# Optimization experiments

Hardware: AMD Instinct MI355X
Metric: run time of the kernel (lower is better)

## Reference

```python
import jax, jax.numpy as jnp
import numpy as np

B, DIM, HEADS, H, W, WS, AWS = 8, 64, 4, 256, 256, 8, 8
HD = DIM // HEADS
SCALE = HD ** -0.5


def _grid_sample_zeros(img, grid):
    # img: (N, C, Hi, Wi); grid: (N, Ho, Wo, 2) with (x, y) in [-1, 1]
    # bilinear, align_corners=True, zero padding (matches F.grid_sample)
    N, C, Hi, Wi = img.shape
    gx = (grid[..., 0] + 1.0) * 0.5 * (Wi - 1)
    gy = (grid[..., 1] + 1.0) * 0.5 * (Hi - 1)
    x0 = jnp.floor(gx).astype(jnp.int32); x1 = x0 + 1
    y0 = jnp.floor(gy).astype(jnp.int32); y1 = y0 + 1
    wx1 = gx - x0; wx0 = 1.0 - wx1
    wy1 = gy - y0; wy0 = 1.0 - wy1

    def one(im, x0, x1, y0, y1, wx0, wx1, wy0, wy1):
        def g(yi, xi):
            valid = ((yi >= 0) & (yi < Hi) & (xi >= 0) & (xi < Wi)).astype(im.dtype)
            v = im[:, jnp.clip(yi, 0, Hi - 1), jnp.clip(xi, 0, Wi - 1)]
            return v * valid[None]
        return (g(y0, x0) * (wy0 * wx0)[None] + g(y0, x1) * (wy0 * wx1)[None]
                + g(y1, x0) * (wy1 * wx0)[None] + g(y1, x1) * (wy1 * wx1)[None])

    return jax.vmap(one)(img, x0, x1, y0, y1, wx0, wx1, wy0, wy1)


def _rel_index():
    c = np.stack(np.meshgrid(np.arange(AWS), np.arange(AWS), indexing='ij'))
    cf = c.reshape(2, -1)
    rel = (cf[:, :, None] - cf[:, None, :]).transpose(1, 2, 0).copy()
    rel[:, :, 0] += AWS - 1
    rel[:, :, 1] += AWS - 1
    rel[:, :, 0] *= 2 * AWS - 1
    return rel.sum(-1)  # (AWS*AWS, AWS*AWS)


_REL_IDX = jnp.asarray(_rel_index())


def setup_inputs():
    key = jax.random.key(0)
    ks = jax.random.split(key, 8)
    s = 0.02
    return {
        'x': jax.random.normal(ks[0], (B, DIM, H, W), jnp.float32),
        'qkv_w': jax.random.normal(ks[1], (3 * DIM, DIM), jnp.float32) * s,
        'qkv_b': jnp.zeros((3 * DIM,), jnp.float32),
        'proj_w': jax.random.normal(ks[2], (DIM, DIM), jnp.float32) * s,
        'proj_b': jnp.zeros((DIM,), jnp.float32),
        'off_w': jax.random.normal(ks[3], (2 * HEADS, DIM), jnp.float32) * s,
        'off_b': jnp.zeros((2 * HEADS,), jnp.float32),
        'sc_w': jax.random.normal(ks[4], (2 * HEADS, DIM), jnp.float32) * s,
        'sc_b': jnp.zeros((2 * HEADS,), jnp.float32),
        'rel_bias': jax.random.normal(ks[5], ((WS + AWS - 1) ** 2, HEADS), jnp.float32) * s,
    }


def reference(x, qkv_w, qkv_b, proj_w, proj_b, off_w, off_b, sc_w, sc_b, rel_bias):
    b, dim, h, w = x.shape
    pad_td = (WS - h % WS) % WS; pad_lr = (WS - w % WS) % WS
    pt, pd = pad_td // 2, pad_td - pad_td // 2
    pl, pr = pad_lr // 2, pad_lr - pad_lr // 2
    eh, ew = h + pad_td, w + pad_lr
    wnh, wnw = eh // WS, ew // WS

    # per-pixel reference grid in [-1,1]; channel 0 = x(w-axis), channel 1 = y(h-axis)
    ref_h = jnp.linspace(-1.0, 1.0, eh)
    ref_w = jnp.linspace(-1.0, 1.0, ew)
    base = jnp.stack([jnp.broadcast_to(ref_w[None, :], (eh, ew)),
                      jnp.broadcast_to(ref_h[:, None], (eh, ew))], 0)
    base = base.reshape(2, wnh, WS, wnw, WS)

    # zero-mean window-relative attention coordinates
    bch = jnp.arange(AWS, dtype=jnp.float32) * 2 * WS / AWS / (eh - 1); bch = bch - bch.mean()
    bcw = jnp.arange(AWS, dtype=jnp.float32) * 2 * WS / AWS / (ew - 1); bcw = bcw - bcw.mean()
    ech = jnp.tile(bch, wnh)
    ecw = jnp.tile(bcw, wnw)
    wc = jnp.stack([jnp.broadcast_to(ecw[None, :], (wnh * AWS, wnw * AWS)),
                    jnp.broadcast_to(ech[:, None], (wnh * AWS, wnw * AWS))], 0)
    wc = wc.reshape(2, wnh, AWS, wnw, AWS)

    xp = jnp.pad(x, ((0, 0), (0, 0), (pt, pd), (pl, pr)))

    # offsets / scales: avgpool(WS) -> leaky_relu -> 1x1 conv
    pooled = xp.reshape(b, dim, wnh, WS, wnw, WS).mean(axis=(3, 5))
    act = jax.nn.leaky_relu(pooled, 0.01)
    off = jnp.einsum('bchw,oc->bohw', act, off_w) + off_b[None, :, None, None]
    off = off.reshape(b * HEADS, 2, wnh, wnw)
    off = off * jnp.array([1.0 / (h // WS), 1.0 / (w // WS)], off.dtype)[None, :, None, None]
    sc = jnp.einsum('bchw,oc->bohw', act, sc_w) + sc_b[None, :, None, None]
    sc = sc.reshape(b * HEADS, 2, wnh, wnw)

    coords = (base[None] + wc[None] * sc[:, :, :, None, :, None]
              + off[:, :, :, None, :, None])  # (b*heads, 2, wnh, AWS, wnw, AWS)
    grid = coords.transpose(0, 2, 3, 4, 5, 1).reshape(b * HEADS, wnh * AWS, wnw * AWS, 2)

    # qkv 1x1 conv, then spatial pad
    qkv = jnp.einsum('bchw,oc->bohw', x, qkv_w) + qkv_b[None, :, None, None]
    qkv = qkv.reshape(b, 3, HEADS, HD, h, w)
    qkv = jnp.pad(qkv, ((0, 0),) * 4 + ((pt, pd), (pl, pr)))
    q = qkv[:, 0].reshape(b * HEADS, HD, eh, ew)
    k = qkv[:, 1].reshape(b * HEADS, HD, eh, ew)
    v = qkv[:, 2].reshape(b * HEADS, HD, eh, ew)

    k_sel = _grid_sample_zeros(k, grid)
    v_sel = _grid_sample_zeros(v, grid)

    q = q.reshape(b, HEADS, HD, wnh, WS, wnw, WS).transpose(0, 3, 5, 1, 4, 6, 2)
    q = q.reshape(b * wnh * wnw, HEADS, WS * WS, HD)

    def to_win(t):
        t = t.reshape(b, HEADS, HD, wnh, AWS, wnw, AWS).transpose(0, 3, 5, 1, 4, 6, 2)
        return t.reshape(b * wnh * wnw, HEADS, AWS * AWS, HD)

    kw, vw = to_win(k_sel), to_win(v_sel)

    dots = jnp.einsum('wnqd,wnkd->wnqk', q, kw) * SCALE
    bias = rel_bias[_REL_IDX]  # (WS*WS, AWS*AWS, HEADS)
    dots = dots + bias.transpose(2, 0, 1)[None]
    attn = jax.nn.softmax(dots, axis=-1)
    out = jnp.einsum('wnqk,wnkd->wnqd', attn, vw)

    out = out.reshape(b, wnh, wnw, HEADS, WS, WS, HD).transpose(0, 3, 6, 1, 4, 2, 5)
    out = out.reshape(b, dim, eh, ew)[:, :, pt:h + pt, pl:w + pl]
    out = jnp.einsum('bchw,oc->bohw', out, proj_w) + proj_b[None, :, None, None]
    return out
```

## Files before the change

### kernel.cpp

```cpp
#include <hip/hip_runtime.h>

#define BATCH 8
#define CDIM 64
#define NHEADS 4
#define HD 16
#define IMG 256
#define WSZ 8
#define WN 32
#define NWIN (WN * WN)

static constexpr size_t OFFSC_FLOATS = (size_t)BATCH * NHEADS * NWIN * 4;
static constexpr size_t MAP_ELEMS = (size_t)BATCH * NHEADS * IMG * IMG * HD;

typedef unsigned short u16;
typedef __attribute__((ext_vector_type(2))) _Float16 h2;
typedef __attribute__((ext_vector_type(8))) _Float16 h8;
typedef __attribute__((ext_vector_type(4))) float f32x4;

__device__ __forceinline__ unsigned cvt_pk_f16(float a, float b) {
    unsigned r;
    asm("v_cvt_pkrtz_f16_f32 %0, %1, %2" : "=v"(r) : "v"(a), "v"(b));
    return r;
}
__device__ __forceinline__ float rcpf(float s) {
    float r;
    asm("v_rcp_f32 %0, %1" : "=v"(r) : "v"(s));
    return r;
}
union UH2 { unsigned u; h2 h; };
__device__ __forceinline__ h2 u2h2(unsigned u) { UH2 x; x.u = u; return x.h; }
__device__ __forceinline__ unsigned h22u(h2 h) { UH2 x; x.h = h; return x.u; }
__device__ __forceinline__ u16 f2h(float f) {
    _Float16 h = (_Float16)f;
    u16 r;
    __builtin_memcpy(&r, &h, 2);
    return r;
}
__device__ __forceinline__ unsigned pk_rne(float a, float b) {
    return (unsigned)f2h(a) | ((unsigned)f2h(b) << 16);
}

#define DPP_RADD(x, ctrl)                                                         \
    x += __int_as_float(__builtin_amdgcn_update_dpp(                              \
        0, __float_as_int(x), (ctrl), 0xF, 0xF, false))

__global__ __launch_bounds__(256) void k_pool(const float* __restrict__ x,
                                              float* __restrict__ actg,
                                              const float* __restrict__ qkv_w,
                                              const float* __restrict__ proj_w,
                                              unsigned* __restrict__ wbf) {
    __shared__ float red[8][8][33];
    int bid = blockIdx.x;
    int cg = bid & 7, wh = (bid >> 3) & 31, b = bid >> 8;
    int t = threadIdx.x;
    int row = t >> 5, colg = t & 31;

    if (bid < 32) {
        int i = bid * 256 + t;
        if (i < 6144) {
            wbf[i] = cvt_pk_f16(qkv_w[2 * i], qkv_w[2 * i + 1]);
        } else {
            int j = i - 6144;
            wbf[i] = cvt_pk_f16(proj_w[2 * j], proj_w[2 * j + 1]);
        }
    }

    const float* xb = x + (((size_t)(b * CDIM + cg * 8) * IMG) + (size_t)(wh * WSZ + row)) * IMG + colg * 8;
    #pragma unroll
    for (int c = 0; c < 8; c++) {
        const float4* p4 = (const float4*)(xb + (size_t)c * IMG * IMG);
        float4 a = p4[0], bq = p4[1];
        red[c][row][colg] = a.x + a.y + a.z + a.w + bq.x + bq.y + bq.z + bq.w;
    }
    __syncthreads();
    int c = t >> 5, ww = t & 31;
    float s = 0.f;
    #pragma unroll
    for (int r = 0; r < 8; r++) s += red[c][r][ww];
    s *= (1.0f / 64.0f);
    s = (s >= 0.f) ? s : 0.01f * s;
    actg[(((size_t)b * CDIM + cg * 8 + c) * WN + wh) * WN + ww] = s;
}

__global__ __launch_bounds__(256) void k_offmv(const float* __restrict__ actg,
                                               const float* __restrict__ off_w,
                                               const float* __restrict__ off_b,
                                               const float* __restrict__ sc_w,
                                               const float* __restrict__ sc_b,
                                               float* __restrict__ offsc) {
    __shared__ float act[CDIM][WN + 1];
    int b = blockIdx.x >> 5, wh = blockIdx.x & 31;
    int t = threadIdx.x;
    for (int i = t; i < CDIM * WN; i += 256) {
        int c = i >> 5, ww = i & 31;
        act[c][ww] = actg[(((size_t)b * CDIM + c) * WN + wh) * WN + ww];
    }
    __syncthreads();
    int ww = t >> 3, oi = t & 7;
    float ao = off_b[oi], as = sc_b[oi];
    #pragma unroll 8
    for (int c = 0; c < CDIM; c++) {
        float av = act[c][ww];
        ao += av * off_w[oi * CDIM + c];
        as += av * sc_w[oi * CDIM + c];
    }
    ao *= (1.0f / 32.0f);
    int n = oi >> 1, d = oi & 1;
    size_t base = (((size_t)(b * NHEADS + n) * NWIN) + wh * WN + ww) << 2;
    offsc[base + d] = ao;
    offsc[base + 2 + d] = as;
}

__global__ __launch_bounds__(256) void k_qkv_mfma(const float* __restrict__ x,
                                                  const u16* __restrict__ wbf,
                                                  const float* __restrict__ qkv_b,
                                                  u16* __restrict__ qm,
                                                  u16* __restrict__ km,
                                                  u16* __restrict__ vm) {
    __shared__ u16 Alds[256 * 64];

    int bid = blockIdx.x;
    bid = (bid & 7) * 256 + (bid >> 3);
    int b = bid >> 8, y = bid & 255;
    int t = threadIdx.x;

    {
        const float* xp = x + ((size_t)b * CDIM * IMG + y) * IMG + t;
        u16* row = Alds + t * 64;
        int sw = t & 7;
        #pragma unroll
        for (int cp = 0; cp < 32; cp++) {
            float a = xp[(size_t)(2 * cp) * IMG * IMG];
            float bq = xp[(size_t)(2 * cp + 1) * IMG * IMG];
            unsigned pk = cvt_pk_f16(a, bq);
            int c = 2 * cp;
            int chunk = c >> 3;
            *(unsigned*)(row + ((chunk ^ sw) << 3) + (c & 7)) = pk;
        }
    }

    int wv = t >> 6, l = t & 63;
    int lr = l & 15, lg = l >> 4;

    h8 afr[4][2];
    #pragma unroll
    for (int pg = 0; pg < 4; pg++) {
        int p = wv * 64 + pg * 16 + lr;
        const u16* prow = Alds + p * 64;
        int psw = p & 7;
        #pragma unroll
        for (int kb = 0; kb < 2; kb++) {
            int chunk = kb * 4 + lg;
            afr[pg][kb] = *(const h8*)(prow + ((chunk ^ psw) << 3));
        }
    }

    u16* const maps[3] = { qm, km, vm };
    #pragma unroll
    for (int ot = 0; ot < 12; ot++) {
        int o = ot * 16 + lr;
        float4 b4 = *(const float4*)(qkv_b + ot * 16 + lg * 4);
        h8 bfr0 = *(const h8*)(wbf + o * 64 + lg * 8);
        h8 bfr1 = *(const h8*)(wbf + o * 64 + 32 + lg * 8);

        f32x4 acc[4];
        #pragma unroll
        for (int pg = 0; pg < 4; pg++) {
            acc[pg] = (f32x4){ b4.x, b4.y, b4.z, b4.w };
            acc[pg] = __builtin_amdgcn_mfma_f32_16x16x32_f16(bfr0, afr[pg][0], acc[pg], 0, 0, 0);
            acc[pg] = __builtin_amdgcn_mfma_f32_16x16x32_f16(bfr1, afr[pg][1], acc[pg], 0, 0, 0);
        }

        u16* mp = maps[ot >> 2];
        int n = ot & 3;
        size_t base = ((size_t)(b * NHEADS + n) * IMG * IMG + (size_t)y * IMG) * HD;
        #pragma unroll
        for (int pg = 0; pg < 4; pg++) {
            size_t sb = base + (size_t)(wv * 64 + pg * 16 + lr) * HD + lg * 4;
            *(uint2*)(mp + sb) = make_uint2(pk_rne(acc[pg][0], acc[pg][1]),
                                            pk_rne(acc[pg][2], acc[pg][3]));
        }
    }
}

__global__ __launch_bounds__(256, 2) void k_attn3(const u16* __restrict__ qm,
                                                  const u16* __restrict__ km,
                                                  const u16* __restrict__ vm,
                                                  const u16* __restrict__ wproj,
                                                  const float* __restrict__ proj_b,
                                                  const float* __restrict__ rel_bias,
                                                  const float* __restrict__ offsc,
                                                  float* __restrict__ out) {
    __shared__ float biasS[NHEADS * 225];
    __shared__ _Float16 hb[NHEADS][2048];
    _Float16* Ob = &hb[0][0];

    int blk = blockIdx.x;
    blk = (blk & 7) * 1024 + (blk >> 3);
    int b = blk >> 10, wh = (blk >> 5) & 31, ww = blk & 31;
    int tid = threadIdx.x, n = tid >> 6, l = tid & 63;
    int g = l >> 4, cl = l & 15;
    int y0 = wh * WSZ, x0 = ww * WSZ;
    const h8 z8 = {};

    for (int i = tid; i < NHEADS * 225; i += 256) {
        int hn = i / 225, idx = i - hn * 225;
        biasS[i] = rel_bias[idx * NHEADS + hn] * 4.0f;
    }

    float4 os4 = *(const float4*)(offsc + ((((size_t)(b * NHEADS + n) * NWIN) + wh * WN + ww) << 2));

    h8 qfr[4];
    {
        const u16* qb = qm + ((size_t)(b * NHEADS + n) << 16) * HD;
        #pragma unroll
        for (int qt = 0; qt < 4; qt++) {
            int q = qt * 16 + cl;
            qfr[qt] = (g < 2)
                ? *(const h8*)(qb + ((size_t)(y0 + (q >> 3)) * IMG + (x0 + (q & 7))) * HD + g * 8)
                : z8;
        }
    }

    h8 wfr[2];
    #pragma unroll
    for (int h = 0; h < 2; h++)
        wfr[h] = *(const h8*)(wproj + (n * 16 + cl) * 64 + h * 32 + g * 8);
    float4 pb4 = *(const float4*)(proj_b + n * 16 + g * 4);

    {
        float offx = os4.x, offy = os4.y;
        float scx = os4.z, scy = os4.w;
        int pi = l >> 3, pj = l & 7;
        float gx = (float)(x0 + pj) + ((float)(2 * pj - 7) * (1.0f / 255.0f) * scx + offx) * 127.5f;
        float gy = (float)(y0 + pi) + ((float)(2 * pi - 7) * (1.0f / 255.0f) * scy + offy) * 127.5f;

        float fx0 = floorf(gx), fy0 = floorf(gy);
        int ix0 = (int)fx0, iy0 = (int)fy0;
        float wx1 = gx - fx0, wx0 = 1.f - wx1;
        float wy1 = gy - fy0, wy0 = 1.f - wy1;

        const u16* kb = km + ((size_t)(b * NHEADS + n) << 16) * HD;
        const u16* vb = vm + ((size_t)(b * NHEADS + n) << 16) * HD;

        int iys[2] = { iy0, iy0 + 1 };
        int ixs[2] = { ix0, ix0 + 1 };
        float wys[2] = { wy0, wy1 };
        float wxs[2] = { wx0, wx1 };

        size_t offs[4];
        h2 w2[4];
        #pragma unroll
        for (int t = 0; t < 4; t++) {
            int yy = iys[t >> 1], xq = ixs[t & 1];
            float wgt = wys[t >> 1] * wxs[t & 1];
            if (yy < 0 || yy >= IMG || xq < 0 || xq >= IMG) wgt = 0.f;
            int yc = min(max(yy, 0), IMG - 1), xc = min(max(xq, 0), IMG - 1);
            offs[t] = ((size_t)yc * IMG + xc) * HD;
            _Float16 hw = (_Float16)wgt;
            w2[t] = (h2){ hw, hw };
        }

        h2 kacc[8], vacc[8];
        #pragma unroll
        for (int i = 0; i < 8; i++) {
            kacc[i] = (h2){ (_Float16)0, (_Float16)0 };
            vacc[i] = (h2){ (_Float16)0, (_Float16)0 };
        }

        {
            uint4 t0[4], t1[4];
            #pragma unroll
            for (int t = 0; t < 4; t++) {
                const uint4* p = (const uint4*)(kb + offs[t]);
                t0[t] = p[0]; t1[t] = p[1];
            }
            #pragma unroll
            for (int t = 0; t < 4; t++) {
                kacc[0] += w2[t] * u2h2(t0[t].x); kacc[1] += w2[t] * u2h2(t0[t].y);
                kacc[2] += w2[t] * u2h2(t0[t].z); kacc[3] += w2[t] * u2h2(t0[t].w);
                kacc[4] += w2[t] * u2h2(t1[t].x); kacc[5] += w2[t] * u2h2(t1[t].y);
                kacc[6] += w2[t] * u2h2(t1[t].z); kacc[7] += w2[t] * u2h2(t1[t].w);
            }
        }
        {
            uint4 t0[4], t1[4];
            #pragma unroll
            for (int t = 0; t < 4; t++) {
                const uint4* p = (const uint4*)(vb + offs[t]);
                t0[t] = p[0]; t1[t] = p[1];
            }
            #pragma unroll
            for (int t = 0; t < 4; t++) {
                vacc[0] += w2[t] * u2h2(t0[t].x); vacc[1] += w2[t] * u2h2(t0[t].y);
                vacc[2] += w2[t] * u2h2(t0[t].z); vacc[3] += w2[t] * u2h2(t0[t].w);
                vacc[4] += w2[t] * u2h2(t1[t].x); vacc[5] += w2[t] * u2h2(t1[t].y);
                vacc[6] += w2[t] * u2h2(t1[t].z); vacc[7] += w2[t] * u2h2(t1[t].w);
            }
        }

        uint4* kp = (uint4*)(&hb[n][0] + (size_t)l * 16);
        kp[0] = make_uint4(h22u(kacc[0]), h22u(kacc[1]), h22u(kacc[2]), h22u(kacc[3]));
        kp[1] = make_uint4(h22u(kacc[4]), h22u(kacc[5]), h22u(kacc[6]), h22u(kacc[7]));

        int p = cl * 4 + g;
        #pragma unroll
        for (int i = 0; i < 8; i++) {
            int d0 = 2 * i, d1 = 2 * i + 1;
            hb[n][1024 + d0 * 64 + (p ^ ((d0 & 3) << 4))] = vacc[i][0];
            hb[n][1024 + d1 * 64 + (p ^ ((d1 & 3) << 4))] = vacc[i][1];
        }
    }

    h8 kfr[4], vfr[2];
    #pragma unroll
    for (int kt = 0; kt < 4; kt++)
        kfr[kt] = (g < 2) ? *(const h8*)(&hb[n][0] + (kt * 16 + cl) * 16 + g * 8) : z8;
    #pragma unroll
    for (int h = 0; h < 2; h++)
        vfr[h] = *(const h8*)(&hb[n][1024] + cl * 64 + ((h * 32 + g * 8) ^ ((cl & 3) << 4)));

    __syncthreads();

    f32x4 dacc[4][4];
    #pragma unroll
    for (int qt = 0; qt < 4; qt++) {
        #pragma unroll
        for (int kt = 0; kt < 4; kt++) {
            int pik = kt * 2 + (cl >> 3), pjk = cl & 7;
            int bidx = n * 225 + (7 - pik) * 15 + (7 - pjk) + (qt * 2 + (g >> 1)) * 15 + (g & 1) * 4;
            f32x4 c = { biasS[bidx], biasS[bidx + 1], biasS[bidx + 2], biasS[bidx + 3] };
            dacc[qt][kt] = __builtin_amdgcn_mfma_f32_16x16x32_f16(qfr[qt], kfr[kt], c, 0, 0, 0);
        }
    }

    _Float16* Pb = &hb[n][0];
    f32x4 oacc[4];
    float inv_[4][4];
    #pragma unroll
    for (int qt = 0; qt < 4; qt++) {
        #pragma unroll
        for (int kt = 0; kt < 4; kt++)
            #pragma unroll
            for (int r = 0; r < 4; r++)
                dacc[qt][kt][r] = exp2f(dacc[qt][kt][r] * 0.36067376f);
        #pragma unroll
        for (int r = 0; r < 4; r++) {
            float s0 = (dacc[qt][0][r] + dacc[qt][1][r]) + (dacc[qt][2][r] + dacc[qt][3][r]);
            DPP_RADD(s0, 0x121);
            DPP_RADD(s0, 0x122);
            DPP_RADD(s0, 0x124);
            DPP_RADD(s0, 0x128);
            inv_[qt][r] = rcpf(s0);
        }
        #pragma unroll
        for (int r = 0; r < 4; r++) {
            unsigned lo = cvt_pk_f16(dacc[qt][0][r], dacc[qt][1][r]);
            unsigned hi = cvt_pk_f16(dacc[qt][2][r], dacc[qt][3][r]);
            *(uint2*)((u16*)Pb + (g * 4 + r) * 64 + ((cl * 4) ^ (r << 4))) = make_uint2(lo, hi);
        }
        f32x4 pv = { 0.f, 0.f, 0.f, 0.f };
        #pragma unroll
        for (int h = 0; h < 2; h++) {
            h8 af = *(const h8*)(Pb + cl * 64 + ((h * 32 + g * 8) ^ ((cl & 3) << 4)));
            pv = __builtin_amdgcn_mfma_f32_16x16x32_f16(af, vfr[h], pv, 0, 0, 0);
        }
        oacc[qt] = pv;
    }

    __syncthreads();

    #pragma unroll
    for (int qt = 0; qt < 4; qt++)
        #pragma unroll
        for (int r = 0; r < 4; r++) {
            int q = qt * 16 + g * 4 + r;
            Ob[q * 64 + ((n * 16 + cl) ^ (g << 4))] = (_Float16)(oacc[qt][r] * inv_[qt][r]);
        }
    __syncthreads();

    #pragma unroll
    for (int qt = 0; qt < 4; qt++) {
        f32x4 pa = { pb4.x, pb4.y, pb4.z, pb4.w };
        #pragma unroll
        for (int h = 0; h < 2; h++) {
            h8 of = *(const h8*)(Ob + (qt * 16 + cl) * 64 + ((h * 32 + g * 8) ^ ((cl >> 2) << 4)));
            pa = __builtin_amdgcn_mfma_f32_16x16x32_f16(wfr[h], of, pa, 0, 0, 0);
        }
        int q = qt * 16 + cl;
        #pragma unroll
        for (int r = 0; r < 4; r++) {
            out[((size_t)(b * CDIM + n * 16 + g * 4 + r) * IMG + y0 + (q >> 3)) * IMG + x0 + (q & 7)] = pa[r];
        }
    }
}

extern "C" void kernel_launch(void* const* d_in, const int* in_sizes, int n_in,
                              void* d_out, int out_size, void* d_ws, size_t ws_size,
                              hipStream_t stream) {
    const float* x      = (const float*)d_in[0];
    const float* qkv_w  = (const float*)d_in[1];
    const float* qkv_b  = (const float*)d_in[2];
    const float* proj_w = (const float*)d_in[3];
    const float* proj_b = (const float*)d_in[4];
    const float* off_w  = (const float*)d_in[5];
    const float* off_b  = (const float*)d_in[6];
    const float* sc_w   = (const float*)d_in[7];
    const float* sc_b   = (const float*)d_in[8];
    const float* rel_b  = (const float*)d_in[9];
    float* out = (float*)d_out;

    float* ws = (float*)d_ws;
    float* offsc = ws;
    u16* wqkv = (u16*)(ws + OFFSC_FLOATS);
    u16* wprj = wqkv + 12288;
    u16* qmm = wprj + 4096;
    u16* kmm = qmm + MAP_ELEMS;
    u16* vmm = kmm + MAP_ELEMS;
    float* actg = (float*)qmm;

    k_pool<<<BATCH * WN * 8, 256, 0, stream>>>(x, actg, qkv_w, proj_w, (unsigned*)wqkv);
    k_offmv<<<BATCH * WN, 256, 0, stream>>>(actg, off_w, off_b, sc_w, sc_b, offsc);
    k_qkv_mfma<<<BATCH * IMG, 256, 0, stream>>>(x, wqkv, qkv_b, qmm, kmm, vmm);
    k_attn3<<<BATCH * NWIN, 256, 0, stream>>>(qmm, kmm, vmm, wprj, proj_b,
                                              rel_b, offsc, out);
}
```

Measured before the change: 225.9 us.

## Process two attention windows per block and prefetch second window's K/V gathers

Each attention block now handles two adjacent 8x8 windows instead of one. Grid size is halved, and the bias table setup and projection weight loads are amortized over both windows. The second window's bilinear K/V gathers and Q loads are issued early, behind sched barriers, so they overlap the first window's softmax and projection work. A separate shared buffer for the output tile is added. This raises register and LDS pressure, which may lower occupancy under launch_bounds(256,2).

Result: slower. 240.8 us (+6.6%).

```diff
diff --git a/kernel.cpp b/kernel.cpp
--- a/kernel.cpp
+++ b/kernel.cpp
@@ -193,14 +193,14 @@
                                                   float* __restrict__ out) {
     __shared__ float biasS[NHEADS * 225];
     __shared__ _Float16 hb[NHEADS][2048];
-    _Float16* Ob = &hb[0][0];
+    __shared__ _Float16 Ob[64 * 64];
 
     int blk = blockIdx.x;
-    blk = (blk & 7) * 1024 + (blk >> 3);
-    int b = blk >> 10, wh = (blk >> 5) & 31, ww = blk & 31;
+    blk = (blk & 7) * 512 + (blk >> 3);
+    int b = blk >> 9, wh = (blk >> 4) & 31, wp = blk & 15;
     int tid = threadIdx.x, n = tid >> 6, l = tid & 63;
     int g = l >> 4, cl = l & 15;
-    int y0 = wh * WSZ, x0 = ww * WSZ;
+    int y0 = wh * WSZ, x0a = wp * 16, x0b = wp * 16 + 8;
     const h8 z8 = {};
 
     for (int i = tid; i < NHEADS * 225; i += 256) {
@@ -208,18 +208,21 @@
         biasS[i] = rel_bias[idx * NHEADS + hn] * 4.0f;
     }
 
-    float4 os4 = *(const float4*)(offsc + ((((size_t)(b * NHEADS + n) * NWIN) + wh * WN + ww) << 2));
-
-    h8 qfr[4];
-    {
-        const u16* qb = qm + ((size_t)(b * NHEADS + n) << 16) * HD;
-        #pragma unroll
-        for (int qt = 0; qt < 4; qt++) {
-            int q = qt * 16 + cl;
-            qfr[qt] = (g < 2)
-                ? *(const h8*)(qb + ((size_t)(y0 + (q >> 3)) * IMG + (x0 + (q & 7))) * HD + g * 8)
-                : z8;
-        }
+    size_t osbase = (((size_t)(b * NHEADS + n) * NWIN) + wh * WN + wp * 2) << 2;
+    float4 osA = *(const float4*)(offsc + osbase);
+    float4 osB = *(const float4*)(offsc + osbase + 4);
+
+    const u16* qb = qm + ((size_t)(b * NHEADS + n) << 16) * HD;
+    const u16* kb = km + ((size_t)(b * NHEADS + n) << 16) * HD;
+    const u16* vb = vm + ((size_t)(b * NHEADS + n) << 16) * HD;
+
+    h8 qfrA[4];
+    #pragma unroll
+    for (int qt = 0; qt < 4; qt++) {
+        int q = qt * 16 + cl;
+        qfrA[qt] = (g < 2)
+            ? *(const h8*)(qb + ((size_t)(y0 + (q >> 3)) * IMG + (x0a + (q & 7))) * HD + g * 8)
+            : z8;
     }
 
     h8 wfr[2];
@@ -229,10 +232,10 @@
     float4 pb4 = *(const float4*)(proj_b + n * 16 + g * 4);
 
     {
-        float offx = os4.x, offy = os4.y;
-        float scx = os4.z, scy = os4.w;
+        float offx = osA.x, offy = osA.y;
+        float scx = osA.z, scy = osA.w;
         int pi = l >> 3, pj = l & 7;
-        float gx = (float)(x0 + pj) + ((float)(2 * pj - 7) * (1.0f / 255.0f) * scx + offx) * 127.5f;
+        float gx = (float)(x0a + pj) + ((float)(2 * pj - 7) * (1.0f / 255.0f) * scx + offx) * 127.5f;
         float gy = (float)(y0 + pi) + ((float)(2 * pi - 7) * (1.0f / 255.0f) * scy + offy) * 127.5f;
 
         float fx0 = floorf(gx), fy0 = floorf(gy);
@@ -240,15 +243,12 @@
         float wx1 = gx - fx0, wx0 = 1.f - wx1;
         float wy1 = gy - fy0, wy0 = 1.f - wy1;
 
-        const u16* kb = km + ((size_t)(b * NHEADS + n) << 16) * HD;
-        const u16* vb = vm + ((size_t)(b * NHEADS + n) << 16) * HD;
-
         int iys[2] = { iy0, iy0 + 1 };
         int ixs[2] = { ix0, ix0 + 1 };
         float wys[2] = { wy0, wy1 };
         float wxs[2] = { wx0, wx1 };
 
-        size_t offs[4];
+        unsigned offs[4];
         h2 w2[4];
         #pragma unroll
         for (int t = 0; t < 4; t++) {
@@ -256,7 +256,7 @@
             float wgt = wys[t >> 1] * wxs[t & 1];
             if (yy < 0 || yy >= IMG || xq < 0 || xq >= IMG) wgt = 0.f;
             int yc = min(max(yy, 0), IMG - 1), xc = min(max(xq, 0), IMG - 1);
-            offs[t] = ((size_t)yc * IMG + xc) * HD;
+            offs[t] = (unsigned)((yc * IMG + xc) * HD);
             _Float16 hw = (_Float16)wgt;
             w2[t] = (h2){ hw, hw };
         }
@@ -322,6 +322,41 @@
 
     __syncthreads();
 
+    unsigned offsB[4];
+    h2 w2B[4];
+    {
+        float offx = osB.x, offy = osB.y;
+        float scx = osB.z, scy = osB.w;
+        int pi = l >> 3, pj = l & 7;
+        float gx = (float)(x0b + pj) + ((float)(2 * pj - 7) * (1.0f / 255.0f) * scx + offx) * 127.5f;
+        float gy = (float)(y0 + pi) + ((float)(2 * pi - 7) * (1.0f / 255.0f) * scy + offy) * 127.5f;
+        float fx0 = floorf(gx), fy0 = floorf(gy);
+        int ix0 = (int)fx0, iy0 = (int)fy0;
+        float wx1 = gx - fx0, wx0 = 1.f - wx1;
+        float wy1 = gy - fy0, wy0 = 1.f - wy1;
+        int iys[2] = { iy0, iy0 + 1 };
+        int ixs[2] = { ix0, ix0 + 1 };
+        float wys[2] = { wy0, wy1 };
+        float wxs[2] = { wx0, wx1 };
+        #pragma unroll
+        for (int t = 0; t < 4; t++) {
+            int yy = iys[t >> 1], xq = ixs[t & 1];
+            float wgt = wys[t >> 1] * wxs[t & 1];
+            if (yy < 0 || yy >= IMG || xq < 0 || xq >= IMG) wgt = 0.f;
+            int yc = min(max(yy, 0), IMG - 1), xc = min(max(xq, 0), IMG - 1);
+            offsB[t] = (unsigned)((yc * IMG + xc) * HD);
+            _Float16 hw = (_Float16)wgt;
+            w2B[t] = (h2){ hw, hw };
+        }
+    }
+    uint4 tp0[4], tp1[4];
+    #pragma unroll
+    for (int t = 0; t < 4; t++) {
+        const uint4* p = (const uint4*)(kb + offsB[t]);
+        tp0[t] = p[0]; tp1[t] = p[1];
+    }
+    __builtin_amdgcn_sched_barrier(0);
+
     f32x4 dacc[4][4];
     #pragma unroll
     for (int qt = 0; qt < 4; qt++) {
@@ -330,7 +365,7 @@
             int pik = kt * 2 + (cl >> 3), pjk = cl & 7;
             int bidx = n * 225 + (7 - pik) * 15 + (7 - pjk) + (qt * 2 + (g >> 1)) * 15 + (g & 1) * 4;
             f32x4 c = { biasS[bidx], biasS[bidx + 1], biasS[bidx + 2], biasS[bidx + 3] };
-            dacc[qt][kt] = __builtin_amdgcn_mfma_f32_16x16x32_f16(qfr[qt], kfr[kt], c, 0, 0, 0);
+            dacc[qt][kt] = __builtin_amdgcn_mfma_f32_16x16x32_f16(qfrA[qt], kfr[kt], c, 0, 0, 0);
         }
     }
 
@@ -368,7 +403,16 @@
         oacc[qt] = pv;
     }
 
-    __syncthreads();
+    h2 kaccB[8];
+    #pragma unroll
+    for (int i = 0; i < 8; i++) kaccB[i] = (h2){ (_Float16)0, (_Float16)0 };
+    #pragma unroll
+    for (int t = 0; t < 4; t++) {
+        kaccB[0] += w2B[t] * u2h2(tp0[t].x); kaccB[1] += w2B[t] * u2h2(tp0[t].y);
+        kaccB[2] += w2B[t] * u2h2(tp0[t].z); kaccB[3] += w2B[t] * u2h2(tp0[t].w);
+        kaccB[4] += w2B[t] * u2h2(tp1[t].x); kaccB[5] += w2B[t] * u2h2(tp1[t].y);
+        kaccB[6] += w2B[t] * u2h2(tp1[t].z); kaccB[7] += w2B[t] * u2h2(tp1[t].w);
+    }
 
     #pragma unroll
     for (int qt = 0; qt < 4; qt++)
@@ -378,6 +422,21 @@
             Ob[q * 64 + ((n * 16 + cl) ^ (g << 4))] = (_Float16)(oacc[qt][r] * inv_[qt][r]);
         }
     __syncthreads();
+
+    #pragma unroll
+    for (int t = 0; t < 4; t++) {
+        const uint4* p = (const uint4*)(vb + offsB[t]);
+        tp0[t] = p[0]; tp1[t] = p[1];
+    }
+    h8 qfrB[4];
+    #pragma unroll
+    for (int qt = 0; qt < 4; qt++) {
+        int q = qt * 16 + cl;
+        qfrB[qt] = (g < 2)
+            ? *(const h8*)(qb + ((size_t)(y0 + (q >> 3)) * IMG + (x0b + (q & 7))) * HD + g * 8)
+            : z8;
+    }
+    __builtin_amdgcn_sched_barrier(0);
 
     #pragma unroll
     for (int qt = 0; qt < 4; qt++) {
@@ -390,7 +449,105 @@
         int q = qt * 16 + cl;
         #pragma unroll
         for (int r = 0; r < 4; r++) {
-            out[((size_t)(b * CDIM + n * 16 + g * 4 + r) * IMG + y0 + (q >> 3)) * IMG + x0 + (q & 7)] = pa[r];
+            out[((size_t)(b * CDIM + n * 16 + g * 4 + r) * IMG + y0 + (q >> 3)) * IMG + x0a + (q & 7)] = pa[r];
+        }
+    }
+
+    {
+        h2 vaccB[8];
+        #pragma unroll
+        for (int i = 0; i < 8; i++) vaccB[i] = (h2){ (_Float16)0, (_Float16)0 };
+        #pragma unroll
+        for (int t = 0; t < 4; t++) {
+            vaccB[0] += w2B[t] * u2h2(tp0[t].x); vaccB[1] += w2B[t] * u2h2(tp0[t].y);
+            vaccB[2] += w2B[t] * u2h2(tp0[t].z); vaccB[3] += w2B[t] * u2h2(tp0[t].w);
+            vaccB[4] += w2B[t] * u2h2(tp1[t].x); vaccB[5] += w2B[t] * u2h2(tp1[t].y);
+            vaccB[6] += w2B[t] * u2h2(tp1[t].z); vaccB[7] += w2B[t] * u2h2(tp1[t].w);
+        }
+
+        uint4* kp = (uint4*)(&hb[n][0] + (size_t)l * 16);
+        kp[0] = make_uint4(h22u(kaccB[0]), h22u(kaccB[1]), h22u(kaccB[2]), h22u(kaccB[3]));
+        kp[1] = make_uint4(h22u(kaccB[4]), h22u(kaccB[5]), h22u(kaccB[6]), h22u(kaccB[7]));
+
+        int p = cl * 4 + g;
+        #pragma unroll
+        for (int i = 0; i < 8; i++) {
+            int d0 = 2 * i, d1 = 2 * i + 1;
+            hb[n][1024 + d0 * 64 + (p ^ ((d0 & 3) << 4))] = vaccB[i][0];
+            hb[n][1024 + d1 * 64 + (p ^ ((d1 & 3) << 4))] = vaccB[i][1];
+        }
+    }
+    #pragma unroll
+    for (int kt = 0; kt < 4; kt++)
+        kfr[kt] = (g < 2) ? *(const h8*)(&hb[n][0] + (kt * 16 + cl) * 16 + g * 8) : z8;
+    #pragma unroll
+    for (int h = 0; h < 2; h++)
+        vfr[h] = *(const h8*)(&hb[n][1024] + cl * 64 + ((h * 32 + g * 8) ^ ((cl & 3) << 4)));
+
+    #pragma unroll
+    for (int qt = 0; qt < 4; qt++) {
+        #pragma unroll
+        for (int kt = 0; kt < 4; kt++) {
+            int pik = kt * 2 + (cl >> 3), pjk = cl & 7;
+            int bidx = n * 225 + (7 - pik) * 15 + (7 - pjk) + (qt * 2 + (g >> 1)) * 15 + (g & 1) * 4;
+            f32x4 c = { biasS[bidx], biasS[bidx + 1], biasS[bidx + 2], biasS[bidx + 3] };
+            dacc[qt][kt] = __builtin_amdgcn_mfma_f32_16x16x32_f16(qfrB[qt], kfr[kt], c, 0, 0, 0);
+        }
+    }
+    #pragma unroll
+    for (int qt = 0; qt < 4; qt++) {
+        #pragma unroll
+        for (int kt = 0; kt < 4; kt++)
+            #pragma unroll
+            for (int r = 0; r < 4; r++)
+                dacc[qt][kt][r] = exp2f(dacc[qt][kt][r] * 0.36067376f);
+        #pragma unroll
+        for (int r = 0; r < 4; r++) {
+            float s0 = (dacc[qt][0][r] + dacc[qt][1][r]) + (dacc[qt][2][r] + dacc[qt][3][r]);
+            DPP_RADD(s0, 0x121);
+            DPP_RADD(s0, 0x122);
+            DPP_RADD(s0, 0x124);
+            DPP_RADD(s0, 0x128);
+            inv_[qt][r] = rcpf(s0);
+        }
+        #pragma unroll
+        for (int r = 0; r < 4; r++) {
+            unsigned lo = cvt_pk_f16(dacc[qt][0][r], dacc[qt][1][r]);
+            unsigned hi = cvt_pk_f16(dacc[qt][2][r], dacc[qt][3][r]);
+            *(uint2*)((u16*)Pb + (g * 4 + r) * 64 + ((cl * 4) ^ (r << 4))) = make_uint2(lo, hi);
+        }
+        f32x4 pv = { 0.f, 0.f, 0.f, 0.f };
+        #pragma unroll
+        for (int h = 0; h < 2; h++) {
+            h8 af = *(const h8*)(Pb + cl * 64 + ((h * 32 + g * 8) ^ ((cl & 3) << 4)));
+            pv = __builtin_amdgcn_mfma_f32_16x16x32_f16(af, vfr[h], pv, 0, 0, 0);
+        }
+        oacc[qt] = pv;
+    }
+
+    __syncthreads();
+
+    #pragma unroll
+    for (int qt = 0; qt < 4; qt++)
+        #pragma unroll
+        for (int r = 0; r < 4; r++) {
+            int q = qt * 16 + g * 4 + r;
+            Ob[q * 64 + ((n * 16 + cl) ^ (g << 4))] = (_Float16)(oacc[qt][r] * inv_[qt][r]);
+        }
+    __syncthreads();
+
+    #pragma unroll
+    for (int qt = 0; qt < 4; qt++) {
+        f32x4 pa = { pb4.x, pb4.y, pb4.z, pb4.w };
+        #pragma unroll
+        for (int h = 0; h < 2; h++) {
+            h8 of = *(const h8*)(Ob + (qt * 16 + cl) * 64 + ((h * 32 + g * 8) ^ ((cl >> 2) << 4)));
+            pa = __builtin_amdgcn_mfma_f32_16x16x32_f16(wfr[h], of, pa, 0, 0, 0);
+        }
+        int q = qt * 16 + cl;
+        #pragma unroll
+        for (int r = 0; r < 4; r++) {
+            out[((size_t)(b * CDIM + n * 16 + g * 4 + r) * IMG + y0 + (q >> 3)) * IMG + x0b + (q & 7)] = pa[r];
         }
     }
 }
@@ -422,6 +579,6 @@
     k_pool<<<BATCH * WN * 8, 256, 0, stream>>>(x, actg, qkv_w, proj_w, (unsigned*)wqkv);
     k_offmv<<<BATCH * WN, 256, 0, stream>>>(actg, off_w, off_b, sc_w, sc_b, offsc);
     k_qkv_mfma<<<BATCH * IMG, 256, 0, stream>>>(x, wqkv, qkv_b, qmm, kmm, vmm);
-    k_attn3<<<BATCH * NWIN, 256, 0, stream>>>(qmm, kmm, vmm, wprj, proj_b,
-                                              rel_b, offsc, out);
-}
+    k_attn3<<<BATCH * NWIN / 2, 256, 0, stream>>>(qmm, kmm, vmm, wprj, proj_b,
+                                                  rel_b, offsc, out);
+}
```
